# Performance work log

Hardware: AMD Instinct MI355X
Metric: run time of the kernel (lower is better)

The kernel has to match this reference:

```python
import jax, jax.numpy as jnp
import numpy as np

B, S, D, H = 2, 2048, 1024, 16
HD = D // H  # head dim = 64
NEG = -1e9


def setup_inputs() -> dict:
    key = jax.random.key(0)
    ks = jax.random.split(key, 8)
    x = jax.random.normal(ks[0], (B, S, D), dtype=jnp.float32)
    mask = jax.random.randint(ks[1], (B, 1, S, S), 0, 2).astype(bool)
    s = 1.0 / np.sqrt(D)
    Wq = jax.random.normal(ks[2], (D, D), dtype=jnp.float32) * s
    bq = jax.random.normal(ks[3], (D,), dtype=jnp.float32) * 0.01
    Wk = jax.random.normal(ks[4], (D, D), dtype=jnp.float32) * s
    bk = jax.random.normal(ks[5], (D,), dtype=jnp.float32) * 0.01
    Wv = jax.random.normal(ks[6], (D, D), dtype=jnp.float32) * s
    bv = jax.random.normal(ks[7], (D,), dtype=jnp.float32) * 0.01
    return {"x": x, "mask": mask, "Wq": Wq, "bq": bq, "Wk": Wk, "bk": bk, "Wv": Wv, "bv": bv}


def reference(x, mask, Wq, bq, Wk, bk, Wv, bv):
    b, s, d = x.shape
    # QKV projections (torch nn.Linear: y = x @ W.T + b)
    q = (x @ Wq.T + bq).reshape(b, s, H, HD).transpose(0, 2, 1, 3)  # [B,H,S,HD]
    k = (x @ Wk.T + bk).reshape(b, s, H, HD).transpose(0, 2, 1, 3)
    v = (x @ Wv.T + bv).reshape(b, s, H, HD).transpose(0, 2, 1, 3)
    # NOTE: original scales by sqrt(hidden_state), not sqrt(head_dim)
    scale = 1.0 / jnp.sqrt(jnp.asarray(d, dtype=x.dtype))
    weight = jnp.einsum('bhqd,bhkd->bhqk', q, k) * scale  # [B,H,S,S]
    weight = jnp.where(mask, jnp.asarray(NEG, dtype=x.dtype), weight)
    score = jax.nn.softmax(weight, axis=-1)
    out = jnp.einsum('bhqk,bhkd->bhqd', score, v)  # [B,H,S,HD]
    return out.transpose(0, 2, 1, 3).reshape(b, s, d)
```

## Files before the change

kernel.cpp:

```cpp
#include <hip/hip_runtime.h>
#include <hip/hip_bf16.h>

typedef __bf16 bf16x8 __attribute__((ext_vector_type(8)));
typedef float f32x4 __attribute__((ext_vector_type(4)));

#define NB 2
#define NS 2048
#define ND 1024
#define NH 16
#define NHD 64

__device__ __forceinline__ unsigned short f2b(float f) {
    union { __hip_bfloat16 h; unsigned short u; } c;
    c.h = __float2bfloat16(f);
    return c.u;
}

__device__ __forceinline__ void gl_lds16(const unsigned short* g, unsigned short* l) {
    __builtin_amdgcn_global_load_lds(
        (const __attribute__((address_space(1))) unsigned int*)g,
        (__attribute__((address_space(3))) unsigned int*)l, 16, 0, 0);
}

__global__ __launch_bounds__(256) void to_bf16_all(
    const float* __restrict__ x,  const float* __restrict__ wq,
    const float* __restrict__ wk, const float* __restrict__ wv,
    unsigned short* __restrict__ xb,  unsigned short* __restrict__ wqb,
    unsigned short* __restrict__ wkb, unsigned short* __restrict__ wvb)
{
    const size_t TX = (size_t)NB * NS * ND / 8;
    const size_t TW = (size_t)ND * ND / 8;
    size_t gid = (size_t)blockIdx.x * 256 + threadIdx.x;
    const float* src; unsigned short* dst; size_t off;
    if (gid < TX)               { src = x;  dst = xb;  off = gid * 8; }
    else if (gid < TX + TW)     { src = wq; dst = wqb; off = (gid - TX) * 8; }
    else if (gid < TX + 2 * TW) { src = wk; dst = wkb; off = (gid - TX - TW) * 8; }
    else                        { src = wv; dst = wvb; off = (gid - TX - 2 * TW) * 8; }
    float4 a = *(const float4*)(src + off);
    float4 b = *(const float4*)(src + off + 4);
    alignas(16) unsigned short t[8];
    t[0] = f2b(a.x); t[1] = f2b(a.y); t[2] = f2b(a.z); t[3] = f2b(a.w);
    t[4] = f2b(b.x); t[5] = f2b(b.y); t[6] = f2b(b.z); t[7] = f2b(b.w);
    *(uint4*)(dst + off) = *(const uint4*)t;
}

__global__ void detect_mask(const unsigned* __restrict__ m, int* __restrict__ flag) {
    __shared__ int bad;
    if (threadIdx.x == 0) bad = 0;
    __syncthreads();
    int mybad = 0;
    for (int i = threadIdx.x; i < 8192; i += 256) {
        unsigned w = m[i];
        if (w != 0u && w != 1u && w != 0x3F800000u) mybad = 1;
    }
    if (mybad) bad = 1;
    __syncthreads();
    if (threadIdx.x == 0) *flag = bad ? 0 : 1;
}

__global__ __launch_bounds__(256) void pack_mask(
    const void* __restrict__ mask, const int* __restrict__ mflag,
    unsigned long long* __restrict__ mbits)
{
    const int wave = threadIdx.x >> 6;
    const int lane = threadIdx.x & 63;
    const size_t w = (size_t)blockIdx.x * 4 + wave;
    const size_t e = w * 64 + lane;
    int v;
    if (*mflag) v = (((const unsigned*)mask)[e] != 0u);
    else        v = (((const unsigned char*)mask)[e] != 0);
    unsigned long long bits = __ballot(v);
    if (lane == 0) mbits[w] = bits;
}

__global__ __launch_bounds__(256) void qkv_gemm(
    const unsigned short* __restrict__ xb,
    const unsigned short* __restrict__ Wqb, const float* __restrict__ bq,
    const unsigned short* __restrict__ Wkb, const float* __restrict__ bk,
    const unsigned short* __restrict__ Wvb, const float* __restrict__ bv,
    unsigned short* __restrict__ Qb, unsigned short* __restrict__ Kb,
    unsigned short* __restrict__ Vtb)
{
    __shared__ alignas(16) unsigned short Alds[128 * 32];
    __shared__ alignas(16) unsigned short Blds[128 * 32];

    const int tid  = threadIdx.x;
    const int wave = tid >> 6;
    const int lane = tid & 63;
    const int z    = blockIdx.z;

    const unsigned short* W = (z == 0) ? Wqb : (z == 1) ? Wkb : Wvb;
    const float* bias       = (z == 0) ? bq  : (z == 1) ? bk  : bv;

    const int m0 = blockIdx.x * 128;
    const int n0 = blockIdx.y * 128;
    const int wr = (wave >> 1) * 64;
    const int wc = (wave & 1) * 64;

    const int r0 = tid >> 2;
    const int r1 = 64 + (tid >> 2);
    const int ss = tid & 3;
    const int aoff0 = r0 * ND + ((ss ^ ((r0 >> 1) & 3)) * 8);
    const int aoff1 = r1 * ND + ((ss ^ ((r1 >> 1) & 3)) * 8);
    unsigned short* ldsA0 = Alds + wave * 512;
    unsigned short* ldsA1 = Alds + 2048 + wave * 512;
    unsigned short* ldsB0 = Blds + wave * 512;
    unsigned short* ldsB1 = Blds + 2048 + wave * 512;

    const unsigned short* xsrc = xb + (size_t)m0 * ND;
    const unsigned short* wsrc = W  + (size_t)n0 * ND;

    const int lg = lane >> 4;
    const int ll = lane & 15;
    const int segb = (lg ^ ((ll >> 1) & 3)) * 16;

    f32x4 acc[4][4] = {};

    for (int kt = 0; kt < ND; kt += 32) {
        if (kt != 0) __syncthreads();
        gl_lds16(xsrc + kt + aoff0, ldsA0);
        gl_lds16(xsrc + kt + aoff1, ldsA1);
        gl_lds16(wsrc + kt + aoff0, ldsB0);
        gl_lds16(wsrc + kt + aoff1, ldsB1);
        __syncthreads();

        bf16x8 af[4], bfr[4];
        #pragma unroll
        for (int m = 0; m < 4; m++)
            af[m] = *(const bf16x8*)((const char*)Alds
                     + (wr + m * 16 + ll) * 64 + segb);
        #pragma unroll
        for (int n = 0; n < 4; n++)
            bfr[n] = *(const bf16x8*)((const char*)Blds
                     + (wc + n * 16 + ll) * 64 + segb);

        #pragma unroll
        for (int m = 0; m < 4; m++)
            #pragma unroll
            for (int n = 0; n < 4; n++)
                acc[m][n] = __builtin_amdgcn_mfma_f32_16x16x32_bf16(
                    af[m], bfr[n], acc[m][n], 0, 0, 0);
    }

    #pragma unroll
    for (int n = 0; n < 4; n++) {
        const int j  = n0 + wc + n * 16 + ll;
        const float bj = bias[j];
        const int hh = j >> 6;
        const int hd = j & 63;
        #pragma unroll
        for (int m = 0; m < 4; m++) {
            #pragma unroll
            for (int r = 0; r < 4; r++) {
                const int i  = m0 + wr + m * 16 + lg * 4 + r;
                const int bb = i >> 11;
                const int sI = i & 2047;
                const unsigned short o = f2b(acc[m][n][r] + bj);
                if (z == 2) {
                    Vtb[((size_t)(bb * NH + hh) * NHD + hd) * NS + sI] = o;
                } else {
                    const size_t idx = ((size_t)(bb * NH + hh) * NS + sI) * NHD + hd;
                    if (z == 0) Qb[idx] = o; else Kb[idx] = o;
                }
            }
        }
    }
}

__global__ __launch_bounds__(512, 4) void attn_kernel(
    const unsigned short* __restrict__ Qb, const unsigned short* __restrict__ Kb,
    const unsigned short* __restrict__ Vtb,
    const unsigned long long* __restrict__ mbits, float* __restrict__ out)
{
    __shared__ alignas(16) unsigned short Kt[64 * 64];
    __shared__ alignas(16) unsigned short Vt[64 * 64];
    __shared__ alignas(16) unsigned short Plds[8][16][72];

    const int tid  = threadIdx.x;
    const int wave = tid >> 6;
    const int lane = tid & 63;

    const int wg   = blockIdx.x;
    const int xcd  = wg & 7;
    const int slot = wg >> 3;
    const int hb   = xcd * 4 + (slot >> 4);
    const int qblk = slot & 15;
    const int h = hb & (NH - 1);
    const int b = hb >> 4;
    const int q0 = qblk * 128 + wave * 16;

    const unsigned short* Qp = Qb  + (size_t)(b * NH + h) * NS * NHD;
    const unsigned short* Kp = Kb  + (size_t)(b * NH + h) * NS * NHD;
    const unsigned short* Vp = Vtb + (size_t)(b * NH + h) * NHD * NS;
    const unsigned long long* mrow = mbits + (size_t)b * NS * (NS / 64);

    const int lg = lane >> 4;
    const int ll = lane & 15;

    const int rw = wave * 8 + (lane >> 3);
    const int sg = (lane & 7) ^ (rw & 7);
    const size_t ksoff = (size_t)rw * NHD + sg * 8;
    const size_t vsoff = (size_t)rw * NS  + sg * 8;
    unsigned short* ldsK = Kt + wave * 512;
    unsigned short* ldsV = Vt + wave * 512;

    const int xr7 = ll & 7;
    const int ka0 = ll * 128 + ((lg)     ^ xr7) * 16;
    const int ka1 = ll * 128 + ((lg + 4) ^ xr7) * 16;

    const int kcol = lg * 8;
    const bf16x8 qf0 = *(const bf16x8*)&Qp[(q0 + ll) * NHD + kcol];
    const bf16x8 qf1 = *(const bf16x8*)&Qp[(q0 + ll) * NHD + 32 + kcol];

    f32x4 O0 = {}, O1 = {}, O2 = {}, O3 = {};
    float mrun = -3.0e38f;
    float lrun = 0.f;

    const float scale = 0.03125f;

    unsigned long long mwc = mrow[(size_t)(q0 + ll) * (NS / 64)];

    for (int t = 0; t < 32; t++) {
        const int kb = t * 64;
        if (t != 0) __syncthreads();
        gl_lds16(Kp + (size_t)kb * NHD + ksoff, ldsK);
        gl_lds16(Vp + kb + vsoff, ldsV);
        const int tn = (t + 1 < 32) ? t + 1 : 0;
        const unsigned long long mwn = mrow[(size_t)(q0 + ll) * (NS / 64) + tn];
        __syncthreads();

        f32x4 s0 = {}, s1 = {}, s2 = {}, s3 = {};
        {
            const bf16x8 k00 = *(const bf16x8*)((const char*)Kt + 0 * 2048 + ka0);
            const bf16x8 k10 = *(const bf16x8*)((const char*)Kt + 1 * 2048 + ka0);
            const bf16x8 k20 = *(const bf16x8*)((const char*)Kt + 2 * 2048 + ka0);
            const bf16x8 k30 = *(const bf16x8*)((const char*)Kt + 3 * 2048 + ka0);
            s0 = __builtin_amdgcn_mfma_f32_16x16x32_bf16(k00, qf0, s0, 0, 0, 0);
            s1 = __builtin_amdgcn_mfma_f32_16x16x32_bf16(k10, qf0, s1, 0, 0, 0);
            s2 = __builtin_amdgcn_mfma_f32_16x16x32_bf16(k20, qf0, s2, 0, 0, 0);
            s3 = __builtin_amdgcn_mfma_f32_16x16x32_bf16(k30, qf0, s3, 0, 0, 0);
            const bf16x8 k01 = *(const bf16x8*)((const char*)Kt + 0 * 2048 + ka1);
            const bf16x8 k11 = *(const bf16x8*)((const char*)Kt + 1 * 2048 + ka1);
            const bf16x8 k21 = *(const bf16x8*)((const char*)Kt + 2 * 2048 + ka1);
            const bf16x8 k31 = *(const bf16x8*)((const char*)Kt + 3 * 2048 + ka1);
            s0 = __builtin_amdgcn_mfma_f32_16x16x32_bf16(k01, qf1, s0, 0, 0, 0);
            s1 = __builtin_amdgcn_mfma_f32_16x16x32_bf16(k11, qf1, s1, 0, 0, 0);
            s2 = __builtin_amdgcn_mfma_f32_16x16x32_bf16(k21, qf1, s2, 0, 0, 0);
            s3 = __builtin_amdgcn_mfma_f32_16x16x32_bf16(k31, qf1, s3, 0, 0, 0);
        }

        const unsigned long long mws = mwc >> (lg * 4);
        float sv[16];
        #pragma unroll
        for (int tt = 0; tt < 4; tt++) {
            const f32x4 st = (tt == 0) ? s0 : (tt == 1) ? s1 : (tt == 2) ? s2 : s3;
            #pragma unroll
            for (int r = 0; r < 4; r++)
                sv[tt * 4 + r] = ((mws >> (16 * tt + r)) & 1ull) ? -1e9f
                                                                 : st[r] * scale;
        }

        float m01 = fmaxf(fmaxf(sv[0], sv[1]), fmaxf(sv[2], sv[3]));
        float m23 = fmaxf(fmaxf(sv[4], sv[5]), fmaxf(sv[6], sv[7]));
        float m45 = fmaxf(fmaxf(sv[8], sv[9]), fmaxf(sv[10], sv[11]));
        float m67 = fmaxf(fmaxf(sv[12], sv[13]), fmaxf(sv[14], sv[15]));
        float mt = fmaxf(fmaxf(m01, m23), fmaxf(m45, m67));
        mt = fmaxf(mt, __shfl_xor(mt, 16));
        mt = fmaxf(mt, __shfl_xor(mt, 32));

        if (!__all(mt <= mrun + 8.0f)) {
            const float mnew  = fmaxf(mrun, mt);
            const float alpha = __expf(mrun - mnew);
            mrun = mnew;
            lrun *= alpha;
            #pragma unroll
            for (int r = 0; r < 4; r++) {
                const float ar = __shfl(alpha, lg * 4 + r);
                O0[r] *= ar; O1[r] *= ar; O2[r] *= ar; O3[r] *= ar;
            }
        }

        float rs = 0.f;
        #pragma unroll
        for (int tt = 0; tt < 4; tt++) {
            const float p0 = __expf(sv[tt * 4 + 0] - mrun);
            const float p1 = __expf(sv[tt * 4 + 1] - mrun);
            const float p2 = __expf(sv[tt * 4 + 2] - mrun);
            const float p3 = __expf(sv[tt * 4 + 3] - mrun);
            rs += (p0 + p1) + (p2 + p3);
            uint2 w;
            w.x = (unsigned)f2b(p0) | ((unsigned)f2b(p1) << 16);
            w.y = (unsigned)f2b(p2) | ((unsigned)f2b(p3) << 16);
            *(uint2*)&Plds[wave][ll][tt * 16 + lg * 4] = w;
        }
        rs += __shfl_xor(rs, 16);
        rs += __shfl_xor(rs, 32);
        lrun += rs;

        const bf16x8 pa0 = *(const bf16x8*)&Plds[wave][ll][kcol];
        const bf16x8 pa1 = *(const bf16x8*)&Plds[wave][ll][32 + kcol];
        {
            const bf16x8 v00 = *(const bf16x8*)((const char*)Vt + 0 * 2048 + ka0);
            const bf16x8 v10 = *(const bf16x8*)((const char*)Vt + 1 * 2048 + ka0);
            const bf16x8 v20 = *(const bf16x8*)((const char*)Vt + 2 * 2048 + ka0);
            const bf16x8 v30 = *(const bf16x8*)((const char*)Vt + 3 * 2048 + ka0);
            O0 = __builtin_amdgcn_mfma_f32_16x16x32_bf16(pa0, v00, O0, 0, 0, 0);
            O1 = __builtin_amdgcn_mfma_f32_16x16x32_bf16(pa0, v10, O1, 0, 0, 0);
            O2 = __builtin_amdgcn_mfma_f32_16x16x32_bf16(pa0, v20, O2, 0, 0, 0);
            O3 = __builtin_amdgcn_mfma_f32_16x16x32_bf16(pa0, v30, O3, 0, 0, 0);
            const bf16x8 v01 = *(const bf16x8*)((const char*)Vt + 0 * 2048 + ka1);
            const bf16x8 v11 = *(const bf16x8*)((const char*)Vt + 1 * 2048 + ka1);
            const bf16x8 v21 = *(const bf16x8*)((const char*)Vt + 2 * 2048 + ka1);
            const bf16x8 v31 = *(const bf16x8*)((const char*)Vt + 3 * 2048 + ka1);
            O0 = __builtin_amdgcn_mfma_f32_16x16x32_bf16(pa1, v01, O0, 0, 0, 0);
            O1 = __builtin_amdgcn_mfma_f32_16x16x32_bf16(pa1, v11, O1, 0, 0, 0);
            O2 = __builtin_amdgcn_mfma_f32_16x16x32_bf16(pa1, v21, O2, 0, 0, 0);
            O3 = __builtin_amdgcn_mfma_f32_16x16x32_bf16(pa1, v31, O3, 0, 0, 0);
        }
        mwc = mwn;
    }

    #pragma unroll
    for (int r = 0; r < 4; r++) {
        const int q = q0 + lg * 4 + r;
        const float inv = 1.0f / __shfl(lrun, lg * 4 + r);
        float* op = out + (size_t)(b * NS + q) * ND + h * NHD;
        op[0 * 16 + ll] = O0[r] * inv;
        op[1 * 16 + ll] = O1[r] * inv;
        op[2 * 16 + ll] = O2[r] * inv;
        op[3 * 16 + ll] = O3[r] * inv;
    }
}

extern "C" void kernel_launch(void* const* d_in, const int* in_sizes, int n_in,
                              void* d_out, int out_size, void* d_ws, size_t ws_size,
                              hipStream_t stream)
{
    const float* x  = (const float*)d_in[0];
    const void* mask = d_in[1];
    const float* Wq = (const float*)d_in[2];
    const float* bq = (const float*)d_in[3];
    const float* Wk = (const float*)d_in[4];
    const float* bk = (const float*)d_in[5];
    const float* Wv = (const float*)d_in[6];
    const float* bv = (const float*)d_in[7];
    float* out = (float*)d_out;

    const size_t szX = (size_t)NB * NS * ND;
    const size_t szW = (size_t)ND * ND;
    const size_t szQ = (size_t)NB * NH * NS * NHD;

    int* mflag = (int*)d_ws;
    unsigned short* xb  = (unsigned short*)((char*)d_ws + 256);
    unsigned short* Wqb = xb  + szX;
    unsigned short* Wkb = Wqb + szW;
    unsigned short* Wvb = Wkb + szW;
    unsigned short* Qb  = Wvb + szW;
    unsigned short* Kb  = Qb + szQ;
    unsigned short* Vtb = Kb + szQ;
    unsigned long long* mbits = (unsigned long long*)(Vtb + szQ);

    dim3 blk(256);
    const int cvtBlocks = (int)((szX + 3 * szW) / 8 / 256);
    to_bf16_all<<<dim3(cvtBlocks), blk, 0, stream>>>(
        x, Wq, Wk, Wv, xb, Wqb, Wkb, Wvb);

    detect_mask<<<dim3(1), blk, 0, stream>>>((const unsigned*)mask, mflag);
    const int words = NB * NS * NS / 64;
    pack_mask<<<dim3(words / 4), blk, 0, stream>>>(mask, mflag, mbits);

    dim3 g1(32, 8, 3);
    qkv_gemm<<<g1, blk, 0, stream>>>(xb, Wqb, bq, Wkb, bk, Wvb, bv, Qb, Kb, Vtb);

    attn_kernel<<<dim3(512), dim3(512), 0, stream>>>(Qb, Kb, Vtb, mbits, out);
}
```

Before: 235.0 us.

## Double QKV GEMM k-tile to 64 and fold softmax scale into Q

The QKV projection GEMM now stages 64-wide K slices per iteration instead of 32, with a new 8-way XOR swizzle on a 128-byte row stride. This halves the number of barrier pairs and load phases per block. Separately, the 1/32 softmax scale is applied when Q is written out, which removes a multiply per score element in the attention loop. The trade-offs are doubled LDS use per GEMM block and Q rounded to bf16 after scaling, a power-of-two factor that should be exact.

```diff
diff --git a/kernel.cpp b/kernel.cpp
--- a/kernel.cpp
+++ b/kernel.cpp
@@ -81,8 +81,8 @@
     unsigned short* __restrict__ Qb, unsigned short* __restrict__ Kb,
     unsigned short* __restrict__ Vtb)
 {
-    __shared__ alignas(16) unsigned short Alds[128 * 32];
-    __shared__ alignas(16) unsigned short Blds[128 * 32];
+    __shared__ alignas(16) unsigned short Alds[128 * 64];
+    __shared__ alignas(16) unsigned short Blds[128 * 64];
 
     const int tid  = threadIdx.x;
     const int wave = tid >> 6;
@@ -97,51 +97,54 @@
     const int wr = (wave >> 1) * 64;
     const int wc = (wave & 1) * 64;
 
-    const int r0 = tid >> 2;
-    const int r1 = 64 + (tid >> 2);
-    const int ss = tid & 3;
-    const int aoff0 = r0 * ND + ((ss ^ ((r0 >> 1) & 3)) * 8);
-    const int aoff1 = r1 * ND + ((ss ^ ((r1 >> 1) & 3)) * 8);
-    unsigned short* ldsA0 = Alds + wave * 512;
-    unsigned short* ldsA1 = Alds + 2048 + wave * 512;
-    unsigned short* ldsB0 = Blds + wave * 512;
-    unsigned short* ldsB1 = Blds + 2048 + wave * 512;
+    int soff[4];
+    #pragma unroll
+    for (int i = 0; i < 4; i++) {
+        const int r = i * 32 + (tid >> 3);
+        soff[i] = r * ND + (((tid & 7) ^ (r & 7)) * 8);
+    }
 
     const unsigned short* xsrc = xb + (size_t)m0 * ND;
     const unsigned short* wsrc = W  + (size_t)n0 * ND;
 
     const int lg = lane >> 4;
     const int ll = lane & 15;
-    const int segb = (lg ^ ((ll >> 1) & 3)) * 16;
+    const int xr7 = ll & 7;
 
     f32x4 acc[4][4] = {};
 
-    for (int kt = 0; kt < ND; kt += 32) {
+    for (int kt = 0; kt < ND; kt += 64) {
         if (kt != 0) __syncthreads();
-        gl_lds16(xsrc + kt + aoff0, ldsA0);
-        gl_lds16(xsrc + kt + aoff1, ldsA1);
-        gl_lds16(wsrc + kt + aoff0, ldsB0);
-        gl_lds16(wsrc + kt + aoff1, ldsB1);
+        #pragma unroll
+        for (int i = 0; i < 4; i++) {
+            gl_lds16(xsrc + kt + soff[i], Alds + i * 2048 + wave * 512);
+            gl_lds16(wsrc + kt + soff[i], Blds + i * 2048 + wave * 512);
+        }
         __syncthreads();
 
-        bf16x8 af[4], bfr[4];
-        #pragma unroll
-        for (int m = 0; m < 4; m++)
-            af[m] = *(const bf16x8*)((const char*)Alds
-                     + (wr + m * 16 + ll) * 64 + segb);
-        #pragma unroll
-        for (int n = 0; n < 4; n++)
-            bfr[n] = *(const bf16x8*)((const char*)Blds
-                     + (wc + n * 16 + ll) * 64 + segb);
-
-        #pragma unroll
-        for (int m = 0; m < 4; m++)
+        #pragma unroll
+        for (int kk = 0; kk < 2; kk++) {
+            const int segb = ((kk * 4 + lg) ^ xr7) * 16;
+            bf16x8 af[4], bfr[4];
+            #pragma unroll
+            for (int m = 0; m < 4; m++)
+                af[m] = *(const bf16x8*)((const char*)Alds
+                         + (wr + m * 16 + ll) * 128 + segb);
             #pragma unroll
             for (int n = 0; n < 4; n++)
-                acc[m][n] = __builtin_amdgcn_mfma_f32_16x16x32_bf16(
-                    af[m], bfr[n], acc[m][n], 0, 0, 0);
-    }
-
+                bfr[n] = *(const bf16x8*)((const char*)Blds
+                         + (wc + n * 16 + ll) * 128 + segb);
+
+            #pragma unroll
+            for (int m = 0; m < 4; m++)
+                #pragma unroll
+                for (int n = 0; n < 4; n++)
+                    acc[m][n] = __builtin_amdgcn_mfma_f32_16x16x32_bf16(
+                        af[m], bfr[n], acc[m][n], 0, 0, 0);
+        }
+    }
+
+    const float oscale = (z == 0) ? 0.03125f : 1.0f;
     #pragma unroll
     for (int n = 0; n < 4; n++) {
         const int j  = n0 + wc + n * 16 + ll;
@@ -155,7 +158,7 @@
                 const int i  = m0 + wr + m * 16 + lg * 4 + r;
                 const int bb = i >> 11;
                 const int sI = i & 2047;
-                const unsigned short o = f2b(acc[m][n][r] + bj);
+                const unsigned short o = f2b((acc[m][n][r] + bj) * oscale);
                 if (z == 2) {
                     Vtb[((size_t)(bb * NH + hh) * NHD + hd) * NS + sI] = o;
                 } else {
@@ -215,8 +218,6 @@
     f32x4 O0 = {}, O1 = {}, O2 = {}, O3 = {};
     float mrun = -3.0e38f;
     float lrun = 0.f;
-
-    const float scale = 0.03125f;
 
     unsigned long long mwc = mrow[(size_t)(q0 + ll) * (NS / 64)];
 
@@ -256,8 +257,7 @@
             const f32x4 st = (tt == 0) ? s0 : (tt == 1) ? s1 : (tt == 2) ? s2 : s3;
             #pragma unroll
             for (int r = 0; r < 4; r++)
-                sv[tt * 4 + r] = ((mws >> (16 * tt + r)) & 1ull) ? -1e9f
-                                                                 : st[r] * scale;
+                sv[tt * 4 + r] = ((mws >> (16 * tt + r)) & 1ull) ? -1e9f : st[r];
         }
 
         float m01 = fmaxf(fmaxf(sv[0], sv[1]), fmaxf(sv[2], sv[3]));
```

Result: no change. 234.4 us (-0.3%).
